# Performance work log

Measured on AMD Instinct MI355X. Metric: run time of the kernel, lower is better.

The kernel has to match this reference:

```python
import jax, jax.numpy as jnp
import numpy as np


def setup_inputs() -> dict:
    key = jax.random.key(0)
    feats = jax.random.normal(key, (16, 64, 128, 128), dtype=jnp.float32)
    return {"feats": feats, "stride": 2}


def reference(feats, stride):
    # Zero-insertion upsampling: equivalent to conv_transpose2d with an
    # s x s kernel whose only nonzero is at [0,0], stride=s, groups=C.
    # out[b,c,i*s,j*s] = feats[b,c,i,j]; all other entries are zero.
    B, C, H, W = feats.shape
    out = jnp.zeros((B, C, H * stride, W * stride), dtype=feats.dtype)
    out = out.at[:, :, ::stride, ::stride].set(feats)
    return out
```

## Files before the change

kernel.cpp:

```cpp
#include <hip/hip_runtime.h>


typedef float f32x4 __attribute__((ext_vector_type(4)));
typedef float f32x2 __attribute__((ext_vector_type(2)));

#define THREADS 256
#define BLOCKS 8192
#define TOTAL_VEC4 16777216u
#define STRIDE (BLOCKS * THREADS)
#define ITERS (TOTAL_VEC4 / STRIDE)

__global__ __launch_bounds__(256) void pad_within_kernel(
    const float* __restrict__ in, float* __restrict__ out) {
    unsigned v0 = blockIdx.x * THREADS + threadIdx.x;
    f32x4* o4 = (f32x4*)out;

    unsigned row0 = v0 >> 6;
    unsigned oh   = row0 & 255u;

    if (oh & 1u) {
        const f32x4 z = {0.f, 0.f, 0.f, 0.f};
#pragma unroll
        for (int k = 0; k < (int)ITERS; ++k) {
            __builtin_nontemporal_store(z, &o4[v0 + (unsigned)k * STRIDE]);
        }
    } else {
        unsigned ih = oh >> 1;
        f32x2 x[ITERS];
#pragma unroll
        for (int k = 0; k < (int)ITERS; ++k) {
            unsigned v    = v0 + (unsigned)k * STRIDE;
            unsigned col4 = v & 63u;
            unsigned bc   = v >> 14;
            const f32x2* irow = (const f32x2*)(in + ((size_t)(bc * 128u + ih)) * 128u);
            x[k] = __builtin_nontemporal_load(&irow[col4]);
        }
#pragma unroll
        for (int k = 0; k < (int)ITERS; ++k) {
            unsigned v = v0 + (unsigned)k * STRIDE;
            f32x4 val = {x[k].x, 0.f, x[k].y, 0.f};
            __builtin_nontemporal_store(val, &o4[v]);
        }
    }
}

extern "C" void kernel_launch(void* const* d_in, const int* in_sizes, int n_in,
                              void* d_out, int out_size, void* d_ws, size_t ws_size,
                              hipStream_t stream) {
    const float* feats = (const float*)d_in[0];
    float* out = (float*)d_out;
    pad_within_kernel<<<dim3(BLOCKS), dim3(THREADS), 0, stream>>>(feats, out);
}
```

Measured before the change: 319.7 us.

## Split upsample into separate zero-odd-rows and fill-even-rows kernels

Replaces the single kernel, whose blocks branch on row parity, with two kernels launched back to back. One writes zeros to all odd output rows and the other copies input into the even rows. This removes per-block branching, gives each kernel a uniform memory pattern, and lets the fill kernel read the input contiguously. In exchange it adds a second launch with a serialization point between them, and the zero kernel's stores are strided at half-row granularity.

```diff
diff --git a/kernel.cpp b/kernel.cpp
--- a/kernel.cpp
+++ b/kernel.cpp
@@ -6,41 +6,44 @@
 
 #define THREADS 256
 #define BLOCKS 8192
-#define TOTAL_VEC4 16777216u
-#define STRIDE (BLOCKS * THREADS)
-#define ITERS (TOTAL_VEC4 / STRIDE)
+#define GRID_THREADS (BLOCKS * THREADS)
+#define HALF_VEC4 8388608u
+#define K_ITERS (HALF_VEC4 / GRID_THREADS)
 
-__global__ __launch_bounds__(256) void pad_within_kernel(
+__global__ __launch_bounds__(256) void zero_odd_rows(float* __restrict__ out) {
+    unsigned v0 = blockIdx.x * THREADS + threadIdx.x;
+    f32x4* o4 = (f32x4*)out;
+    const f32x4 z = {0.f, 0.f, 0.f, 0.f};
+#pragma unroll
+    for (int k = 0; k < (int)K_ITERS; ++k) {
+        unsigned v    = v0 + (unsigned)k * GRID_THREADS;
+        unsigned col4 = v & 63u;
+        unsigned r    = v >> 6;
+        size_t   idx  = (size_t)r * 128 + 64 + col4;
+        __builtin_nontemporal_store(z, &o4[idx]);
+    }
+}
+
+__global__ __launch_bounds__(256) void fill_even_rows(
     const float* __restrict__ in, float* __restrict__ out) {
     unsigned v0 = blockIdx.x * THREADS + threadIdx.x;
     f32x4* o4 = (f32x4*)out;
-
-    unsigned row0 = v0 >> 6;
-    unsigned oh   = row0 & 255u;
-
-    if (oh & 1u) {
-        const f32x4 z = {0.f, 0.f, 0.f, 0.f};
+    const f32x2* i2 = (const f32x2*)in;
+    f32x2 x[K_ITERS];
 #pragma unroll
-        for (int k = 0; k < (int)ITERS; ++k) {
-            __builtin_nontemporal_store(z, &o4[v0 + (unsigned)k * STRIDE]);
-        }
-    } else {
-        unsigned ih = oh >> 1;
-        f32x2 x[ITERS];
+    for (int k = 0; k < (int)K_ITERS; ++k) {
+        unsigned v    = v0 + (unsigned)k * GRID_THREADS;
+        unsigned col4 = v & 63u;
+        unsigned e    = v >> 6;
+        x[k] = __builtin_nontemporal_load(&i2[(size_t)e * 64 + col4]);
+    }
 #pragma unroll
-        for (int k = 0; k < (int)ITERS; ++k) {
-            unsigned v    = v0 + (unsigned)k * STRIDE;
-            unsigned col4 = v & 63u;
-            unsigned bc   = v >> 14;
-            const f32x2* irow = (const f32x2*)(in + ((size_t)(bc * 128u + ih)) * 128u);
-            x[k] = __builtin_nontemporal_load(&irow[col4]);
-        }
-#pragma unroll
-        for (int k = 0; k < (int)ITERS; ++k) {
-            unsigned v = v0 + (unsigned)k * STRIDE;
-            f32x4 val = {x[k].x, 0.f, x[k].y, 0.f};
-            __builtin_nontemporal_store(val, &o4[v]);
-        }
+    for (int k = 0; k < (int)K_ITERS; ++k) {
+        unsigned v    = v0 + (unsigned)k * GRID_THREADS;
+        unsigned col4 = v & 63u;
+        unsigned e    = v >> 6;
+        f32x4 val = {x[k].x, 0.f, x[k].y, 0.f};
+        __builtin_nontemporal_store(val, &o4[(size_t)e * 128 + col4]);
     }
 }
 
@@ -49,5 +52,6 @@
                               hipStream_t stream) {
     const float* feats = (const float*)d_in[0];
     float* out = (float*)d_out;
-    pad_within_kernel<<<dim3(BLOCKS), dim3(THREADS), 0, stream>>>(feats, out);
+    zero_odd_rows<<<dim3(BLOCKS), dim3(THREADS), 0, stream>>>(out);
+    fill_even_rows<<<dim3(BLOCKS), dim3(THREADS), 0, stream>>>(feats, out);
 }
```

After: 305.1 us. 1.05x faster.
